# Optimization experiments

Measured on AMD Instinct MI355X. Metric: run time of the kernel, lower is better.

The kernel has to match this reference:

```python
import jax, jax.numpy as jnp
import numpy as np

EMB_DIM = 1024
NUM_HEAD = 16
HEAD_DIM = EMB_DIM // NUM_HEAD
B, S = 2, 2048


def setup_inputs() -> dict:
    key = jax.random.key(0)
    ks = jax.random.split(key, 10)
    scale = 1.0 / np.sqrt(EMB_DIM)
    x = jax.random.normal(ks[0], (B, S, EMB_DIM), dtype=jnp.float32)
    # causal mask: 1 = keep, 0 = masked out (torch masked_fill(mask == 0, -inf))
    mask = jnp.tril(jnp.ones((S, S), dtype=jnp.int32))[None, None, :, :]
    def lin(kw, kb):
        W = jax.random.uniform(kw, (EMB_DIM, EMB_DIM), jnp.float32, -scale, scale)
        b = jax.random.uniform(kb, (EMB_DIM,), jnp.float32, -scale, scale)
        return W, b
    Wq, bq = lin(ks[1], ks[2])
    Wk, bk = lin(ks[3], ks[4])
    Wv, bv = lin(ks[5], ks[6])
    Wo, bo = lin(ks[7], ks[8])
    return {"x": x, "mask": mask, "Wq": Wq, "bq": bq, "Wk": Wk, "bk": bk,
            "Wv": Wv, "bv": bv, "Wo": Wo, "bo": bo}


def reference(x, mask, Wq, bq, Wk, bk, Wv, bv, Wo, bo):
    Bsz, Sq, _ = x.shape
    # projections; torch Linear: y = x @ W^T + b
    def proj(W, b):
        y = jnp.einsum('bse,fe->bsf', x, W) + b
        return y.reshape(Bsz, Sq, NUM_HEAD, HEAD_DIM).transpose(0, 2, 1, 3)  # [B,H,S,D]
    q = proj(Wq, bq)
    k = proj(Wk, bk)
    v = proj(Wv, bv)
    scaling = jnp.asarray(HEAD_DIM ** 0.5, x.dtype)
    scores = jnp.einsum('bhqd,bhkd->bhqk', q, k) / scaling  # [B,H,S,S]
    scores = jnp.where(mask == 0, -jnp.inf, scores)
    attn = jax.nn.softmax(scores, axis=-1)
    out = jnp.einsum('bhqk,bhkd->bhqd', attn, v)
    out = out.transpose(0, 2, 1, 3).reshape(Bsz, Sq, EMB_DIM)
    return jnp.einsum('bse,fe->bsf', out, Wo) + bo
```

## Files before the change

kernel.cpp:

```cpp
#include <hip/hip_runtime.h>

typedef unsigned short u16;
typedef __attribute__((ext_vector_type(8))) __bf16 bf16x8;
typedef __attribute__((ext_vector_type(8))) short  short8;
typedef __attribute__((ext_vector_type(4))) short  short4v;
typedef __attribute__((ext_vector_type(4))) float  floatx4;

constexpr int Bc = 2, Sc = 2048, Ec = 1024, Hc = 16, Dc = 64;
constexpr int Mc = Bc * Sc;

#define NEG_BIG (-1.0e30f)
#define QSCALE  0.18033688011112042f

__device__ __forceinline__ u16 f2b(float f) {
  union { float f; unsigned u; } c; c.f = f;
  unsigned u = c.u;
  return (u16)((u + 0x7fffu + ((u >> 16) & 1u)) >> 16);
}
__device__ __forceinline__ u16 f2b_fast(float f) {
  union { float f; unsigned u; } c; c.f = f;
  return (u16)((c.u + 0x8000u) >> 16);
}
__device__ __forceinline__ short8 ld8(const u16* p) { return *(const short8*)p; }

__device__ __forceinline__ floatx4 mfma16(short8 a, short8 b, floatx4 c) {
  return __builtin_amdgcn_mfma_f32_16x16x32_bf16(
      __builtin_bit_cast(bf16x8, a), __builtin_bit_cast(bf16x8, b), c, 0, 0, 0);
}

__device__ __forceinline__ void async16(const u16* g, u16* l) {
  __builtin_amdgcn_global_load_lds(
      (const __attribute__((address_space(1))) void*)g,
      (__attribute__((address_space(3))) void*)l, 16, 0, 0);
}

__global__ __launch_bounds__(256) void cvt_kernel(
    const float* __restrict__ x,  const float* __restrict__ Wq,
    const float* __restrict__ Wk, const float* __restrict__ Wv,
    const float* __restrict__ Wo, u16* __restrict__ dst) {
  const size_t i = ((size_t)blockIdx.x * 256 + threadIdx.x) * 4;
  const int seg = (int)(i >> 20);
  const float* src;
  size_t off;
  if (seg < 4)       { src = x;  off = i; }
  else if (seg == 4) { src = Wq; off = i - ((size_t)4 << 20); }
  else if (seg == 5) { src = Wk; off = i - ((size_t)5 << 20); }
  else if (seg == 6) { src = Wv; off = i - ((size_t)6 << 20); }
  else               { src = Wo; off = i - ((size_t)7 << 20); }
  floatx4 v = *(const floatx4*)(src + off);
  short4v o;
  o[0] = (short)f2b(v[0]); o[1] = (short)f2b(v[1]);
  o[2] = (short)f2b(v[2]); o[3] = (short)f2b(v[3]);
  *(short4v*)(dst + i) = o;
}

__device__ __forceinline__ void gemm128(
    const u16* __restrict__ A, const u16* __restrict__ B, int K,
    int m0, int n0, u16* As, u16* Bs, floatx4 acc[4][4]) {
  const int t = threadIdx.x;
  const int w = t >> 6, lane = t & 63;
  const int wm = w & 1, wn = w >> 1;
  const int quad = lane >> 4, l16 = lane & 15;
  const int r = t >> 2;
  const int c = (t & 3) * 8;

#pragma unroll
  for (int i = 0; i < 4; ++i)
#pragma unroll
    for (int j = 0; j < 4; ++j) acc[i][j] = 0.f;

  for (int k0 = 0; k0 < K; k0 += 32) {
#pragma unroll
    for (int jj = 0; jj < 2; ++jj) {
      async16(A + (size_t)(m0 + jj * 64 + r) * K + k0 + c, As + jj * 2048 + w * 512);
      async16(B + (size_t)(n0 + jj * 64 + r) * K + k0 + c, Bs + jj * 2048 + w * 512);
    }
    __syncthreads();
    short8 af[4], bfr[4];
#pragma unroll
    for (int i = 0; i < 4; ++i)
      af[i]  = *(const short8*)(As + (wm * 64 + i * 16 + l16) * 32 + quad * 8);
#pragma unroll
    for (int j = 0; j < 4; ++j)
      bfr[j] = *(const short8*)(Bs + (wn * 64 + j * 16 + l16) * 32 + quad * 8);
#pragma unroll
    for (int i = 0; i < 4; ++i)
#pragma unroll
      for (int j = 0; j < 4; ++j)
        acc[i][j] = mfma16(af[i], bfr[j], acc[i][j]);
    __syncthreads();
  }
}

__global__ __launch_bounds__(256) void qkv_mm(
    const u16* __restrict__ xb, const u16* __restrict__ Wb,
    const float* __restrict__ bq, const float* __restrict__ bk,
    const float* __restrict__ bv,
    u16* __restrict__ Q, u16* __restrict__ K_, u16* __restrict__ Vt) {
  __shared__ __align__(16) u16 As[4096], Bs[4096];
  const int z = blockIdx.z;
  const u16* W = Wb + ((size_t)z << 20);
  const float* bias = (z == 0) ? bq : (z == 1) ? bk : bv;
  const int m0 = blockIdx.y * 128, n0 = blockIdx.x * 128;

  floatx4 acc[4][4];
  gemm128(xb, W, Ec, m0, n0, As, Bs, acc);

  const int t = threadIdx.x, w = t >> 6, lane = t & 63;
  const int wm = w & 1, wn = w >> 1, quad = lane >> 4, l16 = lane & 15;
#pragma unroll
  for (int i = 0; i < 4; ++i)
#pragma unroll
    for (int j = 0; j < 4; ++j)
#pragma unroll
      for (int rr = 0; rr < 4; ++rr) {
        const int row = m0 + wm * 64 + i * 16 + quad * 4 + rr;
        const int col = n0 + wn * 64 + j * 16 + l16;
        float v = acc[i][j][rr] + bias[col];
        if (z == 0) v *= QSCALE;
        const int bb = row >> 11, s = row & (Sc - 1);
        const int h = col >> 6, d = col & (Dc - 1), bh = bb * Hc + h;
        if (z < 2) ((z == 0) ? Q : K_)[((size_t)bh * Sc + s) * Dc + d] = f2b(v);
        else       Vt[((size_t)bh * Dc + d) * Sc + s] = f2b(v);
      }
}

__global__ __launch_bounds__(256) void proj_mm(
    const u16* __restrict__ O, const u16* __restrict__ Wob,
    const float* __restrict__ bias, float* __restrict__ out) {
  __shared__ __align__(16) u16 As[4096], Bs[4096];
  const int m0 = blockIdx.y * 128, n0 = blockIdx.x * 128;

  floatx4 acc[4][4];
  gemm128(O, Wob, Ec, m0, n0, As, Bs, acc);

  const int t = threadIdx.x, w = t >> 6, lane = t & 63;
  const int wm = w & 1, wn = w >> 1, quad = lane >> 4, l16 = lane & 15;
#pragma unroll
  for (int i = 0; i < 4; ++i)
#pragma unroll
    for (int j = 0; j < 4; ++j)
#pragma unroll
      for (int rr = 0; rr < 4; ++rr) {
        const int row = m0 + wm * 64 + i * 16 + quad * 4 + rr;
        const int col = n0 + wn * 64 + j * 16 + l16;
        out[(size_t)row * Ec + col] = acc[i][j][rr] + bias[col];
      }
}

__global__ __launch_bounds__(256, 4) void attn_kernel(
    const u16* __restrict__ Q, const u16* __restrict__ K,
    const u16* __restrict__ Vt, u16* __restrict__ O) {
  const int qt = 31 - (int)((blockIdx.x + blockIdx.y) & 31);
  const int q0 = qt * 64;
  const int bh = blockIdx.y;
  const int bb = bh >> 4, h = bh & 15;

  const u16* Qh = Q  + (size_t)bh * Sc * Dc;
  const u16* Kh = K  + (size_t)bh * Sc * Dc;
  const u16* Vh = Vt + (size_t)bh * Dc * Sc;

  const int t = threadIdx.x;
  const int w = t >> 6, lane = t & 63;
  const int quad = lane >> 4, l16 = lane & 15;

  __shared__ __align__(16) u16 Ks[8192];
  __shared__ __align__(16) u16 Vs[8192];
  __shared__ __align__(16) u16 Pl[4096];
  u16* const Pw = Pl + w * 1024;

  const int sr = w * 8 + (lane >> 3);
  const int sb = (lane & 7) ^ (lane >> 3);
  const int swz = l16 & 7;

  const u16* qrow_p = Qh + (size_t)(q0 + w * 16 + l16) * Dc;
  const short8 aq0 = ld8(qrow_p + quad * 8);
  const short8 aq1 = ld8(qrow_p + 32 + quad * 8);

  float   lrow[4];
  floatx4 oacc[4];
#pragma unroll
  for (int r = 0; r < 4; ++r) lrow[r] = 0.f;
#pragma unroll
  for (int dt = 0; dt < 4; ++dt) oacc[dt] = 0.f;

  for (int kt = 0; kt <= q0; kt += 128) {
#pragma unroll
    for (int st = 0; st < 2; ++st)
#pragma unroll
      for (int it = 0; it < 2; ++it) {
        const int r = it * 32 + sr;
        async16(Kh + (size_t)(kt + st * 64 + r) * Dc + sb * 8,
                Ks + st * 4096 + it * 2048 + w * 512);
        async16(Vh + (size_t)r * Sc + kt + st * 64 + sb * 8,
                Vs + st * 4096 + it * 2048 + w * 512);
      }
    __syncthreads();

    floatx4 sacc[8];
#pragma unroll
    for (int nt = 0; nt < 8; ++nt) sacc[nt] = 0.f;
#pragma unroll
    for (int ks = 0; ks < 2; ++ks) {
      const short8 a = ks ? aq1 : aq0;
#pragma unroll
      for (int nt = 0; nt < 8; ++nt) {
        const short8 b = *(const short8*)(
            Ks + (nt >> 2) * 4096 + ((nt & 3) * 16 + l16) * 64 +
            (((ks * 4 + quad) ^ swz) * 8));
        sacc[nt] = mfma16(a, b, sacc[nt]);
      }
    }

    const bool diag = (kt + 128 > q0);
    float s2buf[4][4];
#pragma unroll
    for (int r = 0; r < 4; ++r) {
      const int row = quad * 4 + r;
      float sv[8];
#pragma unroll
      for (int nt = 0; nt < 8; ++nt) sv[nt] = sacc[nt][r];
      if (diag) {
        const int qrow = q0 + w * 16 + row;
#pragma unroll
        for (int nt = 0; nt < 8; ++nt)
          if (kt + nt * 16 + l16 > qrow) sv[nt] = NEG_BIG;
      }
      float ls = 0.f;
#pragma unroll
      for (int nt = 0; nt < 8; ++nt) {
        const float pv = exp2f(sv[nt]);
        sv[nt] = pv;
        ls += pv;
      }
      lrow[r] += ls;
      const int sx = row & 7;
#pragma unroll
      for (int j = 0; j < 4; ++j) {
        Pw[row * 64 + (((2 * j + (l16 >> 3)) ^ sx) * 8) + (l16 & 7)] =
            f2b_fast(sv[j]);
        s2buf[r][j] = sv[4 + j];
      }
    }

#pragma unroll
    for (int kc = 0; kc < 2; ++kc) {
      const short8 a = ld8(Pw + l16 * 64 + (((kc * 4 + quad) ^ swz) * 8));
#pragma unroll
      for (int dt = 0; dt < 4; ++dt) {
        const short8 b = *(const short8*)(
            Vs + (dt * 16 + l16) * 64 + (((kc * 4 + quad) ^ swz) * 8));
        oacc[dt] = mfma16(a, b, oacc[dt]);
      }
    }

#pragma unroll
    for (int r = 0; r < 4; ++r) {
      const int row = quad * 4 + r, sx = row & 7;
#pragma unroll
      for (int j = 0; j < 4; ++j)
        Pw[row * 64 + (((2 * j + (l16 >> 3)) ^ sx) * 8) + (l16 & 7)] =
            f2b_fast(s2buf[r][j]);
    }

#pragma unroll
    for (int kc = 0; kc < 2; ++kc) {
      const short8 a = ld8(Pw + l16 * 64 + (((kc * 4 + quad) ^ swz) * 8));
#pragma unroll
      for (int dt = 0; dt < 4; ++dt) {
        const short8 b = *(const short8*)(
            Vs + 4096 + (dt * 16 + l16) * 64 + (((kc * 4 + quad) ^ swz) * 8));
        oacc[dt] = mfma16(a, b, oacc[dt]);
      }
    }
    __syncthreads();
  }

#pragma unroll
  for (int r = 0; r < 4; ++r)
#pragma unroll
    for (int sh = 1; sh < 16; sh <<= 1) lrow[r] += __shfl_xor(lrow[r], sh, 16);

#pragma unroll
  for (int dt = 0; dt < 4; ++dt) {
#pragma unroll
    for (int r = 0; r < 4; ++r) {
      const int qrow = q0 + w * 16 + quad * 4 + r;
      const float ov = oacc[dt][r] / lrow[r];
      O[((size_t)(bb * Sc + qrow)) * Ec + h * Dc + dt * 16 + l16] = f2b(ov);
    }
  }
}

extern "C" void kernel_launch(void* const* d_in, const int* in_sizes, int n_in,
                              void* d_out, int out_size, void* d_ws, size_t ws_size,
                              hipStream_t stream) {
  const float* x  = (const float*)d_in[0];
  const float* Wq = (const float*)d_in[2];
  const float* bq = (const float*)d_in[3];
  const float* Wk = (const float*)d_in[4];
  const float* bk = (const float*)d_in[5];
  const float* Wv = (const float*)d_in[6];
  const float* bv = (const float*)d_in[7];
  const float* Wo = (const float*)d_in[8];
  const float* bo = (const float*)d_in[9];

  const size_t MiE = (size_t)Mc * Ec;
  u16* Q  = (u16*)d_ws;
  u16* K  = Q  + MiE;
  u16* Vt = K  + MiE;
  u16* O  = Vt + MiE;
  u16* xb = O  + MiE;
  u16* Wb = xb + MiE;
  u16* Wob = Wb + ((size_t)3 << 20);

  cvt_kernel<<<8192, 256, 0, stream>>>(x, Wq, Wk, Wv, Wo, xb);
  qkv_mm<<<dim3(Ec / 128, Mc / 128, 3), 256, 0, stream>>>(
      xb, Wb, bq, bk, bv, Q, K, Vt);
  attn_kernel<<<dim3(32, Bc * Hc), 256, 0, stream>>>(Q, K, Vt, O);
  proj_mm<<<dim3(Ec / 128, Mc / 128), 256, 0, stream>>>(O, Wob, bo, (float*)d_out);
}
```

Baseline: 214.2 us.

## Compute transposed scores to keep P in registers and permute V layout

The QK^T MFMA now takes K as the A operand and Q as the B operand, so each lane holds a column of scores in the layout the PV MFMA expects for its A operand. P is packed to bf16 with v_cvt_pk_bf16_f32 and fed directly, which removes the LDS round trip for P and its buffer. To match this, V is stored with a permuted sequence index during the QKV projection. Masking becomes a zeroing of probabilities, row sums are reduced with fewer shuffles, and the grid is remapped so blocks of different causal lengths mix across heads. The risks are extra register pressure from holding P and the tight coupling between the V permutation and the MFMA operand layout.

New measurement: 202.0 us. 1.06x faster.

```diff
diff --git a/kernel.cpp b/kernel.cpp
--- a/kernel.cpp
+++ b/kernel.cpp
@@ -5,11 +5,11 @@
 typedef __attribute__((ext_vector_type(8))) short  short8;
 typedef __attribute__((ext_vector_type(4))) short  short4v;
 typedef __attribute__((ext_vector_type(4))) float  floatx4;
+typedef __attribute__((ext_vector_type(4))) int    intx4;
 
 constexpr int Bc = 2, Sc = 2048, Ec = 1024, Hc = 16, Dc = 64;
 constexpr int Mc = Bc * Sc;
 
-#define NEG_BIG (-1.0e30f)
 #define QSCALE  0.18033688011112042f
 
 __device__ __forceinline__ u16 f2b(float f) {
@@ -17,11 +17,13 @@
   unsigned u = c.u;
   return (u16)((u + 0x7fffu + ((u >> 16) & 1u)) >> 16);
 }
-__device__ __forceinline__ u16 f2b_fast(float f) {
-  union { float f; unsigned u; } c; c.f = f;
-  return (u16)((c.u + 0x8000u) >> 16);
-}
 __device__ __forceinline__ short8 ld8(const u16* p) { return *(const short8*)p; }
+
+__device__ __forceinline__ int cvt_pk(float lo, float hi) {
+  int r;
+  asm("v_cvt_pk_bf16_f32 %0, %1, %2" : "=v"(r) : "v"(lo), "v"(hi));
+  return r;
+}
 
 __device__ __forceinline__ floatx4 mfma16(short8 a, short8 b, floatx4 c) {
   return __builtin_amdgcn_mfma_f32_16x16x32_bf16(
@@ -121,7 +123,10 @@
         const int bb = row >> 11, s = row & (Sc - 1);
         const int h = col >> 6, d = col & (Dc - 1), bh = bb * Hc + h;
         if (z < 2) ((z == 0) ? Q : K_)[((size_t)bh * Sc + s) * Dc + d] = f2b(v);
-        else       Vt[((size_t)bh * Dc + d) * Sc + s] = f2b(v);
+        else {
+          const int sp = (s & ~31) | ((s & 12) << 1) | ((s & 16) >> 2) | (s & 3);
+          Vt[((size_t)bh * Dc + d) * Sc + sp] = f2b(v);
+        }
       }
 }
 
@@ -151,9 +156,11 @@
 __global__ __launch_bounds__(256, 4) void attn_kernel(
     const u16* __restrict__ Q, const u16* __restrict__ K,
     const u16* __restrict__ Vt, u16* __restrict__ O) {
-  const int qt = 31 - (int)((blockIdx.x + blockIdx.y) & 31);
+  const int v  = blockIdx.x & 31, g8 = blockIdx.x >> 5, kk = blockIdx.y;
+  const int q1 = (kk & 2) ? ((v + 8) & 31) : v;
+  const int qt = (kk & 1) ? (31 - q1) : q1;
   const int q0 = qt * 64;
-  const int bh = blockIdx.y;
+  const int bh = kk * 8 + g8;
   const int bb = bh >> 4, h = bh & 15;
 
   const u16* Qh = Q  + (size_t)bh * Sc * Dc;
@@ -166,8 +173,6 @@
 
   __shared__ __align__(16) u16 Ks[8192];
   __shared__ __align__(16) u16 Vs[8192];
-  __shared__ __align__(16) u16 Pl[4096];
-  u16* const Pw = Pl + w * 1024;
 
   const int sr = w * 8 + (lane >> 3);
   const int sb = (lane & 7) ^ (lane >> 3);
@@ -177,10 +182,8 @@
   const short8 aq0 = ld8(qrow_p + quad * 8);
   const short8 aq1 = ld8(qrow_p + 32 + quad * 8);
 
-  float   lrow[4];
+  float   lrow = 0.f;
   floatx4 oacc[4];
-#pragma unroll
-  for (int r = 0; r < 4; ++r) lrow[r] = 0.f;
 #pragma unroll
   for (int dt = 0; dt < 4; ++dt) oacc[dt] = 0.f;
 
@@ -199,95 +202,70 @@
 
     floatx4 sacc[8];
 #pragma unroll
-    for (int nt = 0; nt < 8; ++nt) sacc[nt] = 0.f;
+    for (int g = 0; g < 8; ++g) sacc[g] = 0.f;
 #pragma unroll
     for (int ks = 0; ks < 2; ++ks) {
-      const short8 a = ks ? aq1 : aq0;
-#pragma unroll
-      for (int nt = 0; nt < 8; ++nt) {
-        const short8 b = *(const short8*)(
-            Ks + (nt >> 2) * 4096 + ((nt & 3) * 16 + l16) * 64 +
+      const short8 bq = ks ? aq1 : aq0;
+#pragma unroll
+      for (int g = 0; g < 8; ++g) {
+        const short8 a = *(const short8*)(
+            Ks + (g >> 2) * 4096 + ((g & 3) * 16 + l16) * 64 +
             (((ks * 4 + quad) ^ swz) * 8));
-        sacc[nt] = mfma16(a, b, sacc[nt]);
+        sacc[g] = mfma16(a, bq, sacc[g]);
       }
     }
 
     const bool diag = (kt + 128 > q0);
-    float s2buf[4][4];
-#pragma unroll
-    for (int r = 0; r < 4; ++r) {
-      const int row = quad * 4 + r;
-      float sv[8];
-#pragma unroll
-      for (int nt = 0; nt < 8; ++nt) sv[nt] = sacc[nt][r];
-      if (diag) {
-        const int qrow = q0 + w * 16 + row;
-#pragma unroll
-        for (int nt = 0; nt < 8; ++nt)
-          if (kt + nt * 16 + l16 > qrow) sv[nt] = NEG_BIG;
-      }
-      float ls = 0.f;
-#pragma unroll
-      for (int nt = 0; nt < 8; ++nt) {
-        const float pv = exp2f(sv[nt]);
-        sv[nt] = pv;
-        ls += pv;
-      }
-      lrow[r] += ls;
-      const int sx = row & 7;
-#pragma unroll
-      for (int j = 0; j < 4; ++j) {
-        Pw[row * 64 + (((2 * j + (l16 >> 3)) ^ sx) * 8) + (l16 & 7)] =
-            f2b_fast(sv[j]);
-        s2buf[r][j] = sv[4 + j];
-      }
-    }
-
-#pragma unroll
-    for (int kc = 0; kc < 2; ++kc) {
-      const short8 a = ld8(Pw + l16 * 64 + (((kc * 4 + quad) ^ swz) * 8));
+    const int thr = q0 + w * 16 + l16 - kt - 4 * quad;
+#pragma unroll
+    for (int g = 0; g < 8; ++g)
+#pragma unroll
+      for (int r = 0; r < 4; ++r) {
+        float pv = exp2f(sacc[g][r]);
+        if (diag && (16 * g + r > thr)) pv = 0.f;
+        lrow += pv;
+        sacc[g][r] = pv;
+      }
+
+    short8 pa[4];
+#pragma unroll
+    for (int c = 0; c < 4; ++c) {
+      intx4 wd;
+      wd[0] = cvt_pk(sacc[2 * c][0],     sacc[2 * c][1]);
+      wd[1] = cvt_pk(sacc[2 * c][2],     sacc[2 * c][3]);
+      wd[2] = cvt_pk(sacc[2 * c + 1][0], sacc[2 * c + 1][1]);
+      wd[3] = cvt_pk(sacc[2 * c + 1][2], sacc[2 * c + 1][3]);
+      pa[c] = __builtin_bit_cast(short8, wd);
+    }
+
+#pragma unroll
+    for (int c = 0; c < 4; ++c) {
+      const int st = c >> 1, kcl = c & 1;
 #pragma unroll
       for (int dt = 0; dt < 4; ++dt) {
         const short8 b = *(const short8*)(
-            Vs + (dt * 16 + l16) * 64 + (((kc * 4 + quad) ^ swz) * 8));
-        oacc[dt] = mfma16(a, b, oacc[dt]);
-      }
-    }
-
-#pragma unroll
-    for (int r = 0; r < 4; ++r) {
-      const int row = quad * 4 + r, sx = row & 7;
-#pragma unroll
-      for (int j = 0; j < 4; ++j)
-        Pw[row * 64 + (((2 * j + (l16 >> 3)) ^ sx) * 8) + (l16 & 7)] =
-            f2b_fast(s2buf[r][j]);
-    }
-
-#pragma unroll
-    for (int kc = 0; kc < 2; ++kc) {
-      const short8 a = ld8(Pw + l16 * 64 + (((kc * 4 + quad) ^ swz) * 8));
-#pragma unroll
-      for (int dt = 0; dt < 4; ++dt) {
-        const short8 b = *(const short8*)(
-            Vs + 4096 + (dt * 16 + l16) * 64 + (((kc * 4 + quad) ^ swz) * 8));
-        oacc[dt] = mfma16(a, b, oacc[dt]);
+            Vs + st * 4096 + (dt * 16 + l16) * 64 +
+            (((kcl * 4 + quad) ^ swz) * 8));
+        oacc[dt] = mfma16(pa[c], b, oacc[dt]);
       }
     }
     __syncthreads();
   }
 
+  lrow += __shfl_xor(lrow, 16);
+  lrow += __shfl_xor(lrow, 32);
+  float rs[4];
 #pragma unroll
   for (int r = 0; r < 4; ++r)
-#pragma unroll
-    for (int sh = 1; sh < 16; sh <<= 1) lrow[r] += __shfl_xor(lrow[r], sh, 16);
+    rs[r] = 1.f / __shfl(lrow, quad * 4 + r, 16);
 
 #pragma unroll
   for (int dt = 0; dt < 4; ++dt) {
 #pragma unroll
     for (int r = 0; r < 4; ++r) {
       const int qrow = q0 + w * 16 + quad * 4 + r;
-      const float ov = oacc[dt][r] / lrow[r];
-      O[((size_t)(bb * Sc + qrow)) * Ec + h * Dc + dt * 16 + l16] = f2b(ov);
+      O[((size_t)(bb * Sc + qrow)) * Ec + h * Dc + dt * 16 + l16] =
+          f2b(oacc[dt][r] * rs[r]);
     }
   }
 }
@@ -317,6 +295,6 @@
   cvt_kernel<<<8192, 256, 0, stream>>>(x, Wq, Wk, Wv, Wo, xb);
   qkv_mm<<<dim3(Ec / 128, Mc / 128, 3), 256, 0, stream>>>(
       xb, Wb, bq, bk, bv, Q, K, Vt);
-  attn_kernel<<<dim3(32, Bc * Hc), 256, 0, stream>>>(Q, K, Vt, O);
+  attn_kernel<<<dim3(256, 4), 256, 0, stream>>>(Q, K, Vt, O);
   proj_mm<<<dim3(Ec / 128, Mc / 128), 256, 0, stream>>>(O, Wob, bo, (float*)d_out);
 }
```
